# Performance work log

Measured on AMD Instinct MI355X. Metric: run time of the kernel, lower is better.

The kernel has to match this reference:

```python
import jax, jax.numpy as jnp
import numpy as np

C = 256
R = 16
K = 7

def setup_inputs() -> dict:
    key = jax.random.key(0)
    k1, k2, k3, k4 = jax.random.split(key, 4)
    x = jax.random.normal(k1, (16, C, 128, 128), dtype=jnp.float32)
    # PyTorch Linear weights: w1 [C//R, C], w2 [C, C//R]
    w1 = jax.random.normal(k2, (C // R, C), dtype=jnp.float32) * (1.0 / np.sqrt(C))
    w2 = jax.random.normal(k3, (C, C // R), dtype=jnp.float32) * (1.0 / np.sqrt(C // R))
    # Conv2d(2,1,K) weight: [out=1, in=2, K, K]
    wconv = jax.random.normal(k4, (1, 2, K, K), dtype=jnp.float32) * (1.0 / np.sqrt(2 * K * K))
    return {"x": x, "w1": w1, "w2": w2, "wconv": wconv}

def _mlp(v, w1, w2):  # v: [B, C]
    h = jax.nn.relu(v @ w1.T)  # [B, C//R]
    return h @ w2.T            # [B, C]

def reference(x, w1, w2, wconv):
    # channel attention
    avg = jnp.mean(x, axis=(2, 3))  # [B, C]
    mx = jnp.max(x, axis=(2, 3))    # [B, C]
    ch_att = jax.nn.sigmoid(_mlp(avg, w1, w2) + _mlp(mx, w1, w2))  # [B, C]
    x = x * ch_att[:, :, None, None]
    # spatial attention
    avg_sp = jnp.mean(x, axis=1, keepdims=True)  # [B,1,H,W]
    max_sp = jnp.max(x, axis=1, keepdims=True)   # [B,1,H,W]
    sp = jnp.concatenate([avg_sp, max_sp], axis=1)  # [B,2,H,W]
    conv = jax.lax.conv_general_dilated(
        sp, wconv, window_strides=(1, 1), padding=[(K // 2, K // 2)] * 2,
        dimension_numbers=("NCHW", "OIHW", "NCHW"))  # [B,1,H,W]
    sp_att = jax.nn.sigmoid(conv)
    return x * sp_att
```

## Files before the change

### kernel.cpp

```cpp
#include <hip/hip_runtime.h>
#include <hip/hip_fp16.h>
#include <math.h>

#define B   16
#define C   256
#define HW  16384
#define HW4 4096
#define HW8 2048
#define NCHUNK 4

typedef float vf4 __attribute__((ext_vector_type(4)));
typedef unsigned int vu4 __attribute__((ext_vector_type(4)));
typedef unsigned int vu2 __attribute__((ext_vector_type(2)));

__device__ __forceinline__ float2 h2f(unsigned int w) {
    __half2 h = *(const __half2*)&w;
    return __half22float2(h);
}

__device__ __forceinline__ float wave_reduce_sum(float v) {
    #pragma unroll
    for (int o = 32; o > 0; o >>= 1) v += __shfl_down(v, o, 64);
    return v;
}
__device__ __forceinline__ float wave_reduce_max(float v) {
    #pragma unroll
    for (int o = 32; o > 0; o >>= 1) v = fmaxf(v, __shfl_down(v, o, 64));
    return v;
}

__global__ __launch_bounds__(256) void k_chan_stats_cast(const float* __restrict__ x,
                                                         vu2* __restrict__ x16,
                                                         float* __restrict__ avg,
                                                         float* __restrict__ mx) {
    const int bc  = blockIdx.x;
    const int tid = threadIdx.x;
    const vf4* x4 = (const vf4*)x + (size_t)bc * HW4;
    vu2* o = x16 + (size_t)bc * HW4;
    float s = 0.f, m = -INFINITY;
    #pragma unroll
    for (int i = 0; i < 16; ++i) {
        vf4 v = __builtin_nontemporal_load(&x4[tid + i * 256]);
        s += (v.x + v.y) + (v.z + v.w);
        m = fmaxf(m, fmaxf(fmaxf(v.x, v.y), fmaxf(v.z, v.w)));
        __half2 lo = __halves2half2(__float2half_rn(v.x), __float2half_rn(v.y));
        __half2 hi = __halves2half2(__float2half_rn(v.z), __float2half_rn(v.w));
        vu2 u;
        u.x = *(const unsigned int*)&lo;
        u.y = *(const unsigned int*)&hi;
        o[tid + i * 256] = u;
    }
    s = wave_reduce_sum(s);
    m = wave_reduce_max(m);
    __shared__ float ss[4], sm[4];
    const int wid = tid >> 6, lane = tid & 63;
    if (lane == 0) { ss[wid] = s; sm[wid] = m; }
    __syncthreads();
    if (tid == 0) {
        float S = ss[0] + ss[1] + ss[2] + ss[3];
        float M = fmaxf(fmaxf(sm[0], sm[1]), fmaxf(sm[2], sm[3]));
        avg[bc] = S * (1.0f / HW);
        mx[bc]  = M;
    }
}

__global__ __launch_bounds__(256) void k_mlp(const float* __restrict__ avg,
                                             const float* __restrict__ mx,
                                             const float* __restrict__ w1,
                                             const float* __restrict__ w2,
                                             float* __restrict__ chatt) {
    const int b = blockIdx.x, tid = threadIdx.x;
    __shared__ float sa[C], sx[C], h[16];
    sa[tid] = avg[b * C + tid];
    sx[tid] = mx[b * C + tid];
    __syncthreads();
    const int j = tid >> 4, sub = tid & 15;
    float pa = 0.f, pm = 0.f;
    #pragma unroll
    for (int c2 = sub; c2 < C; c2 += 16) {
        float w = w1[j * C + c2];
        pa += sa[c2] * w;
        pm += sx[c2] * w;
    }
    #pragma unroll
    for (int o = 8; o > 0; o >>= 1) {
        pa += __shfl_down(pa, o, 16);
        pm += __shfl_down(pm, o, 16);
    }
    if (sub == 0) h[j] = fmaxf(pa, 0.f) + fmaxf(pm, 0.f);
    __syncthreads();
    float o = 0.f;
    #pragma unroll
    for (int jj = 0; jj < 16; ++jj) o += h[jj] * w2[tid * 16 + jj];
    chatt[b * C + tid] = 1.0f / (1.0f + expf(-o));
}

__global__ __launch_bounds__(256) void k_sp_partial(const vu4* __restrict__ x16,
                                                    const float* __restrict__ chatt,
                                                    float* __restrict__ pavg,
                                                    float* __restrict__ pmax) {
    const int blk   = blockIdx.x;
    const int chunk = blk & 3;
    const int tile  = (blk >> 2) & 7;
    const int b     = blk >> 5;
    const int tid   = threadIdx.x;
    const int g     = tile * 256 + tid;
    float s[8];
    float m[8];
    #pragma unroll
    for (int k = 0; k < 8; ++k) { s[k] = 0.f; m[k] = -INFINITY; }
    const int c0 = chunk * 64;
    #pragma unroll 4
    for (int c = c0; c < c0 + 64; ++c) {
        vu4 u = x16[((size_t)(b * C + c)) * HW8 + g];
        const float a = chatt[b * C + c];
        #pragma unroll
        for (int q = 0; q < 4; ++q) {
            float2 f = h2f(u[q]);
            float y0 = f.x * a, y1 = f.y * a;
            s[2*q]   += y0;  s[2*q+1] += y1;
            m[2*q]   = fmaxf(m[2*q],   y0);
            m[2*q+1] = fmaxf(m[2*q+1], y1);
        }
    }
    vf4* pa = (vf4*)(pavg + ((size_t)(chunk * B + b)) * HW + g * 8);
    vf4* pm = (vf4*)(pmax + ((size_t)(chunk * B + b)) * HW + g * 8);
    vf4 a0 = {s[0], s[1], s[2], s[3]};
    vf4 a1 = {s[4], s[5], s[6], s[7]};
    vf4 m0 = {m[0], m[1], m[2], m[3]};
    vf4 m1 = {m[4], m[5], m[6], m[7]};
    pa[0] = a0; pa[1] = a1;
    pm[0] = m0; pm[1] = m1;
}

__global__ __launch_bounds__(256) void k_comb_conv(const float* __restrict__ pavg,
                                                   const float* __restrict__ pmax,
                                                   const float* __restrict__ wc,
                                                   float* __restrict__ spatt) {
    const int blk = blockIdx.x;
    const int tx = blk & 7, ty = (blk >> 3) & 7, b = blk >> 6;
    __shared__ float sa[22][24], sm[22][24], swc[98];
    if (threadIdx.x < 98) swc[threadIdx.x] = wc[threadIdx.x];
    for (int idx = threadIdx.x; idx < 484; idx += 256) {
        const int ly = idx / 22, lx = idx - ly * 22;
        const int gy = ty * 16 + ly - 3, gx = tx * 16 + lx - 3;
        float s = 0.f, m = 0.f;
        if (gy >= 0 && gy < 128 && gx >= 0 && gx < 128) {
            const int p = gy * 128 + gx;
            float mm = -INFINITY;
            float ss = 0.f;
            #pragma unroll
            for (int ch = 0; ch < NCHUNK; ++ch) {
                ss += pavg[(size_t)(ch * B + b) * HW + p];
                mm = fmaxf(mm, pmax[(size_t)(ch * B + b) * HW + p]);
            }
            s = ss * (1.0f / C);
            m = mm;
        }
        sa[ly][lx] = s;
        sm[ly][lx] = m;
    }
    __syncthreads();
    const int px = threadIdx.x & 15, py = threadIdx.x >> 4;
    float acc = 0.f;
    #pragma unroll
    for (int kh = 0; kh < 7; ++kh) {
        #pragma unroll
        for (int kw = 0; kw < 7; ++kw) {
            acc += sa[py + kh][px + kw] * swc[kh * 7 + kw]
                 + sm[py + kh][px + kw] * swc[49 + kh * 7 + kw];
        }
    }
    spatt[(size_t)b * HW + (ty * 16 + py) * 128 + tx * 16 + px] =
        1.0f / (1.0f + expf(-acc));
}

__global__ __launch_bounds__(256) void k_final(const vu4* __restrict__ x16,
                                               const float* __restrict__ chatt,
                                               const vf4* __restrict__ spatt,
                                               vf4* __restrict__ out) {
    const size_t total  = (size_t)B * C * HW8;
    const size_t stride = (size_t)gridDim.x * 256;
    for (size_t f = (size_t)blockIdx.x * 256 + threadIdx.x; f < total; f += stride) {
        const size_t bc = f >> 11;
        const size_t g  = f & 2047;
        const size_t b  = bc >> 8;
        vu4 u = __builtin_nontemporal_load(&x16[f]);
        const float a = chatt[bc];
        vf4 sp0 = spatt[b * HW4 + g * 2];
        vf4 sp1 = spatt[b * HW4 + g * 2 + 1];
        float2 f0 = h2f(u.x);
        float2 f1 = h2f(u.y);
        float2 f2 = h2f(u.z);
        float2 f3 = h2f(u.w);
        vf4 r0, r1;
        r0.x = f0.x * a * sp0.x;  r0.y = f0.y * a * sp0.y;
        r0.z = f1.x * a * sp0.z;  r0.w = f1.y * a * sp0.w;
        r1.x = f2.x * a * sp1.x;  r1.y = f2.y * a * sp1.y;
        r1.z = f3.x * a * sp1.z;  r1.w = f3.y * a * sp1.w;
        __builtin_nontemporal_store(r0, &out[f * 2]);
        __builtin_nontemporal_store(r1, &out[f * 2 + 1]);
    }
}

extern "C" void kernel_launch(void* const* d_in, const int* in_sizes, int n_in,
                              void* d_out, int out_size, void* d_ws, size_t ws_size,
                              hipStream_t stream) {
    const float* x  = (const float*)d_in[0];
    const float* w1 = (const float*)d_in[1];
    const float* w2 = (const float*)d_in[2];
    const float* wc = (const float*)d_in[3];
    vf4* out = (vf4*)d_out;
    char* ws = (char*)d_ws;

    vu2* x16  = (vu2*)ws;
    char* p = ws + (size_t)B * C * HW * 2;
    float* avg   = (float*)p;            p += 4096 * 4;
    float* mx    = (float*)p;            p += 4096 * 4;
    float* chatt = (float*)p;            p += 4096 * 4;
    float* pavg  = (float*)p;            p += (size_t)NCHUNK * B * HW * 4;
    float* pmax  = (float*)p;            p += (size_t)NCHUNK * B * HW * 4;
    float* spatt = (float*)p;            p += (size_t)B * HW * 4;

    k_chan_stats_cast<<<B * C, 256, 0, stream>>>(x, x16, avg, mx);
    k_mlp<<<B, 256, 0, stream>>>(avg, mx, w1, w2, chatt);
    k_sp_partial<<<512, 256, 0, stream>>>((const vu4*)x16, chatt, pavg, pmax);
    k_comb_conv<<<1024, 256, 0, stream>>>(pavg, pmax, wc, spatt);
    k_final<<<4096, 256, 0, stream>>>((const vu4*)x16, chatt,
                                      (const vf4*)spatt, (vf4*)out);
}
```

Before: 209.8 us.

## Fuse all CBAM stages into one persistent kernel with grid barriers

```diff
diff --git a/kernel.cpp b/kernel.cpp
--- a/kernel.cpp
+++ b/kernel.cpp
@@ -8,6 +8,7 @@
 #define HW4 4096
 #define HW8 2048
 #define NCHUNK 4
+#define NBLK 512
 
 typedef float vf4 __attribute__((ext_vector_type(4)));
 typedef unsigned int vu4 __attribute__((ext_vector_type(4)));
@@ -29,177 +30,203 @@
     return v;
 }
 
-__global__ __launch_bounds__(256) void k_chan_stats_cast(const float* __restrict__ x,
-                                                         vu2* __restrict__ x16,
-                                                         float* __restrict__ avg,
-                                                         float* __restrict__ mx) {
-    const int bc  = blockIdx.x;
+__device__ __forceinline__ void gbar(unsigned* bar) {
+    __syncthreads();
+    if (threadIdx.x == 0) {
+        __threadfence();
+        unsigned g = __hip_atomic_load(&bar[32], __ATOMIC_RELAXED, __HIP_MEMORY_SCOPE_AGENT);
+        unsigned a = __hip_atomic_fetch_add(&bar[0], 1u, __ATOMIC_ACQ_REL, __HIP_MEMORY_SCOPE_AGENT);
+        if (a == NBLK - 1) {
+            __hip_atomic_store(&bar[0], 0u, __ATOMIC_RELAXED, __HIP_MEMORY_SCOPE_AGENT);
+            __hip_atomic_store(&bar[32], g + 1u, __ATOMIC_RELEASE, __HIP_MEMORY_SCOPE_AGENT);
+        } else {
+            while (__hip_atomic_load(&bar[32], __ATOMIC_ACQUIRE, __HIP_MEMORY_SCOPE_AGENT) == g)
+                __builtin_amdgcn_s_sleep(2);
+        }
+        __threadfence();
+    }
+    __syncthreads();
+}
+
+__global__ __launch_bounds__(256, 2) void k_cbam_fused(
+        const float* __restrict__ x,
+        const float* __restrict__ w1,
+        const float* __restrict__ w2,
+        const float* __restrict__ wc,
+        vu2*  __restrict__ x16,
+        float* __restrict__ avg, float* __restrict__ mx,
+        float* __restrict__ chatt,
+        float* __restrict__ pavg, float* __restrict__ pmax,
+        float* __restrict__ spatt,
+        vf4* __restrict__ out,
+        unsigned* __restrict__ bar) {
     const int tid = threadIdx.x;
-    const vf4* x4 = (const vf4*)x + (size_t)bc * HW4;
-    vu2* o = x16 + (size_t)bc * HW4;
-    float s = 0.f, m = -INFINITY;
-    #pragma unroll
-    for (int i = 0; i < 16; ++i) {
-        vf4 v = __builtin_nontemporal_load(&x4[tid + i * 256]);
-        s += (v.x + v.y) + (v.z + v.w);
-        m = fmaxf(m, fmaxf(fmaxf(v.x, v.y), fmaxf(v.z, v.w)));
-        __half2 lo = __halves2half2(__float2half_rn(v.x), __float2half_rn(v.y));
-        __half2 hi = __halves2half2(__float2half_rn(v.z), __float2half_rn(v.w));
-        vu2 u;
-        u.x = *(const unsigned int*)&lo;
-        u.y = *(const unsigned int*)&hi;
-        o[tid + i * 256] = u;
-    }
-    s = wave_reduce_sum(s);
-    m = wave_reduce_max(m);
-    __shared__ float ss[4], sm[4];
-    const int wid = tid >> 6, lane = tid & 63;
-    if (lane == 0) { ss[wid] = s; sm[wid] = m; }
-    __syncthreads();
-    if (tid == 0) {
-        float S = ss[0] + ss[1] + ss[2] + ss[3];
-        float M = fmaxf(fmaxf(sm[0], sm[1]), fmaxf(sm[2], sm[3]));
-        avg[bc] = S * (1.0f / HW);
-        mx[bc]  = M;
-    }
-}
-
-__global__ __launch_bounds__(256) void k_mlp(const float* __restrict__ avg,
-                                             const float* __restrict__ mx,
-                                             const float* __restrict__ w1,
-                                             const float* __restrict__ w2,
-                                             float* __restrict__ chatt) {
-    const int b = blockIdx.x, tid = threadIdx.x;
-    __shared__ float sa[C], sx[C], h[16];
-    sa[tid] = avg[b * C + tid];
-    sx[tid] = mx[b * C + tid];
-    __syncthreads();
-    const int j = tid >> 4, sub = tid & 15;
-    float pa = 0.f, pm = 0.f;
-    #pragma unroll
-    for (int c2 = sub; c2 < C; c2 += 16) {
-        float w = w1[j * C + c2];
-        pa += sa[c2] * w;
-        pm += sx[c2] * w;
-    }
-    #pragma unroll
-    for (int o = 8; o > 0; o >>= 1) {
-        pa += __shfl_down(pa, o, 16);
-        pm += __shfl_down(pm, o, 16);
-    }
-    if (sub == 0) h[j] = fmaxf(pa, 0.f) + fmaxf(pm, 0.f);
-    __syncthreads();
-    float o = 0.f;
-    #pragma unroll
-    for (int jj = 0; jj < 16; ++jj) o += h[jj] * w2[tid * 16 + jj];
-    chatt[b * C + tid] = 1.0f / (1.0f + expf(-o));
-}
-
-__global__ __launch_bounds__(256) void k_sp_partial(const vu4* __restrict__ x16,
-                                                    const float* __restrict__ chatt,
-                                                    float* __restrict__ pavg,
-                                                    float* __restrict__ pmax) {
-    const int blk   = blockIdx.x;
-    const int chunk = blk & 3;
-    const int tile  = (blk >> 2) & 7;
-    const int b     = blk >> 5;
-    const int tid   = threadIdx.x;
-    const int g     = tile * 256 + tid;
-    float s[8];
-    float m[8];
-    #pragma unroll
-    for (int k = 0; k < 8; ++k) { s[k] = 0.f; m[k] = -INFINITY; }
-    const int c0 = chunk * 64;
-    #pragma unroll 4
-    for (int c = c0; c < c0 + 64; ++c) {
-        vu4 u = x16[((size_t)(b * C + c)) * HW8 + g];
-        const float a = chatt[b * C + c];
-        #pragma unroll
-        for (int q = 0; q < 4; ++q) {
-            float2 f = h2f(u[q]);
-            float y0 = f.x * a, y1 = f.y * a;
-            s[2*q]   += y0;  s[2*q+1] += y1;
-            m[2*q]   = fmaxf(m[2*q],   y0);
-            m[2*q+1] = fmaxf(m[2*q+1], y1);
-        }
-    }
-    vf4* pa = (vf4*)(pavg + ((size_t)(chunk * B + b)) * HW + g * 8);
-    vf4* pm = (vf4*)(pmax + ((size_t)(chunk * B + b)) * HW + g * 8);
-    vf4 a0 = {s[0], s[1], s[2], s[3]};
-    vf4 a1 = {s[4], s[5], s[6], s[7]};
-    vf4 m0 = {m[0], m[1], m[2], m[3]};
-    vf4 m1 = {m[4], m[5], m[6], m[7]};
-    pa[0] = a0; pa[1] = a1;
-    pm[0] = m0; pm[1] = m1;
-}
-
-__global__ __launch_bounds__(256) void k_comb_conv(const float* __restrict__ pavg,
-                                                   const float* __restrict__ pmax,
-                                                   const float* __restrict__ wc,
-                                                   float* __restrict__ spatt) {
     const int blk = blockIdx.x;
-    const int tx = blk & 7, ty = (blk >> 3) & 7, b = blk >> 6;
-    __shared__ float sa[22][24], sm[22][24], swc[98];
-    if (threadIdx.x < 98) swc[threadIdx.x] = wc[threadIdx.x];
-    for (int idx = threadIdx.x; idx < 484; idx += 256) {
-        const int ly = idx / 22, lx = idx - ly * 22;
-        const int gy = ty * 16 + ly - 3, gx = tx * 16 + lx - 3;
-        float s = 0.f, m = 0.f;
-        if (gy >= 0 && gy < 128 && gx >= 0 && gx < 128) {
-            const int p = gy * 128 + gx;
-            float mm = -INFINITY;
-            float ss = 0.f;
+
+    __shared__ union {
+        struct { float sa[22][24]; float sm[22][24]; float wcs[98]; } conv;
+        struct { float sa[C]; float sx[C]; float h[16]; } mlp;
+        struct { float ss[4]; float sm[4]; } red;
+    } sh;
+
+    for (int k = 0; k < 8; ++k) {
+        const int bc = blk + k * NBLK;
+        const vf4* x4 = (const vf4*)x + (size_t)bc * HW4;
+        vu2* o = x16 + (size_t)bc * HW4;
+        float s = 0.f, m = -INFINITY;
+        #pragma unroll
+        for (int i = 0; i < 16; ++i) {
+            vf4 v = __builtin_nontemporal_load(&x4[tid + i * 256]);
+            s += (v.x + v.y) + (v.z + v.w);
+            m = fmaxf(m, fmaxf(fmaxf(v.x, v.y), fmaxf(v.z, v.w)));
+            __half2 lo = __halves2half2(__float2half_rn(v.x), __float2half_rn(v.y));
+            __half2 hi = __halves2half2(__float2half_rn(v.z), __float2half_rn(v.w));
+            vu2 u;
+            u.x = *(const unsigned int*)&lo;
+            u.y = *(const unsigned int*)&hi;
+            o[tid + i * 256] = u;
+        }
+        s = wave_reduce_sum(s);
+        m = wave_reduce_max(m);
+        const int wid = tid >> 6, lane = tid & 63;
+        if (lane == 0) { sh.red.ss[wid] = s; sh.red.sm[wid] = m; }
+        __syncthreads();
+        if (tid == 0) {
+            float S = sh.red.ss[0] + sh.red.ss[1] + sh.red.ss[2] + sh.red.ss[3];
+            float M = fmaxf(fmaxf(sh.red.sm[0], sh.red.sm[1]),
+                            fmaxf(sh.red.sm[2], sh.red.sm[3]));
+            avg[bc] = S * (1.0f / HW);
+            mx[bc]  = M;
+        }
+        __syncthreads();
+    }
+    gbar(bar);
+
+    if (blk < B) {
+        const int b = blk;
+        sh.mlp.sa[tid] = avg[b * C + tid];
+        sh.mlp.sx[tid] = mx[b * C + tid];
+        __syncthreads();
+        const int j = tid >> 4, sub = tid & 15;
+        float pa = 0.f, pm = 0.f;
+        #pragma unroll
+        for (int c2 = sub; c2 < C; c2 += 16) {
+            float w = w1[j * C + c2];
+            pa += sh.mlp.sa[c2] * w;
+            pm += sh.mlp.sx[c2] * w;
+        }
+        #pragma unroll
+        for (int o = 8; o > 0; o >>= 1) {
+            pa += __shfl_down(pa, o, 16);
+            pm += __shfl_down(pm, o, 16);
+        }
+        if (sub == 0) sh.mlp.h[j] = fmaxf(pa, 0.f) + fmaxf(pm, 0.f);
+        __syncthreads();
+        float o = 0.f;
+        #pragma unroll
+        for (int jj = 0; jj < 16; ++jj) o += sh.mlp.h[jj] * w2[tid * 16 + jj];
+        chatt[b * C + tid] = 1.0f / (1.0f + expf(-o));
+    }
+    gbar(bar);
+
+    {
+        const int chunk = blk & 3;
+        const int tile  = (blk >> 2) & 7;
+        const int b     = blk >> 5;
+        const int g     = tile * 256 + tid;
+        const vu4* xx = (const vu4*)x16;
+        float s[8], m[8];
+        #pragma unroll
+        for (int k = 0; k < 8; ++k) { s[k] = 0.f; m[k] = -INFINITY; }
+        const int c0 = chunk * 64;
+        #pragma unroll 4
+        for (int c = c0; c < c0 + 64; ++c) {
+            vu4 u = xx[((size_t)(b * C + c)) * HW8 + g];
+            const float a = chatt[b * C + c];
             #pragma unroll
-            for (int ch = 0; ch < NCHUNK; ++ch) {
-                ss += pavg[(size_t)(ch * B + b) * HW + p];
-                mm = fmaxf(mm, pmax[(size_t)(ch * B + b) * HW + p]);
+            for (int q = 0; q < 4; ++q) {
+                float2 f = h2f(u[q]);
+                float y0 = f.x * a, y1 = f.y * a;
+                s[2*q]   += y0;  s[2*q+1] += y1;
+                m[2*q]   = fmaxf(m[2*q],   y0);
+                m[2*q+1] = fmaxf(m[2*q+1], y1);
             }
-            s = ss * (1.0f / C);
-            m = mm;
-        }
-        sa[ly][lx] = s;
-        sm[ly][lx] = m;
-    }
-    __syncthreads();
-    const int px = threadIdx.x & 15, py = threadIdx.x >> 4;
-    float acc = 0.f;
-    #pragma unroll
-    for (int kh = 0; kh < 7; ++kh) {
-        #pragma unroll
-        for (int kw = 0; kw < 7; ++kw) {
-            acc += sa[py + kh][px + kw] * swc[kh * 7 + kw]
-                 + sm[py + kh][px + kw] * swc[49 + kh * 7 + kw];
-        }
-    }
-    spatt[(size_t)b * HW + (ty * 16 + py) * 128 + tx * 16 + px] =
-        1.0f / (1.0f + expf(-acc));
-}
-
-__global__ __launch_bounds__(256) void k_final(const vu4* __restrict__ x16,
-                                               const float* __restrict__ chatt,
-                                               const vf4* __restrict__ spatt,
-                                               vf4* __restrict__ out) {
-    const size_t total  = (size_t)B * C * HW8;
-    const size_t stride = (size_t)gridDim.x * 256;
-    for (size_t f = (size_t)blockIdx.x * 256 + threadIdx.x; f < total; f += stride) {
-        const size_t bc = f >> 11;
-        const size_t g  = f & 2047;
-        const size_t b  = bc >> 8;
-        vu4 u = __builtin_nontemporal_load(&x16[f]);
-        const float a = chatt[bc];
-        vf4 sp0 = spatt[b * HW4 + g * 2];
-        vf4 sp1 = spatt[b * HW4 + g * 2 + 1];
-        float2 f0 = h2f(u.x);
-        float2 f1 = h2f(u.y);
-        float2 f2 = h2f(u.z);
-        float2 f3 = h2f(u.w);
-        vf4 r0, r1;
-        r0.x = f0.x * a * sp0.x;  r0.y = f0.y * a * sp0.y;
-        r0.z = f1.x * a * sp0.z;  r0.w = f1.y * a * sp0.w;
-        r1.x = f2.x * a * sp1.x;  r1.y = f2.y * a * sp1.y;
-        r1.z = f3.x * a * sp1.z;  r1.w = f3.y * a * sp1.w;
-        __builtin_nontemporal_store(r0, &out[f * 2]);
-        __builtin_nontemporal_store(r1, &out[f * 2 + 1]);
+        }
+        vf4* pa = (vf4*)(pavg + ((size_t)(chunk * B + b)) * HW + g * 8);
+        vf4* pm = (vf4*)(pmax + ((size_t)(chunk * B + b)) * HW + g * 8);
+        vf4 a0 = {s[0], s[1], s[2], s[3]};
+        vf4 a1 = {s[4], s[5], s[6], s[7]};
+        vf4 m0 = {m[0], m[1], m[2], m[3]};
+        vf4 m1 = {m[4], m[5], m[6], m[7]};
+        pa[0] = a0; pa[1] = a1;
+        pm[0] = m0; pm[1] = m1;
+    }
+    gbar(bar);
+
+    for (int t = 0; t < 2; ++t) {
+        const int tj = blk + t * NBLK;
+        const int tx = tj & 7, ty = (tj >> 3) & 7, b = tj >> 6;
+        if (tid < 98) sh.conv.wcs[tid] = wc[tid];
+        for (int idx = tid; idx < 484; idx += 256) {
+            const int ly = idx / 22, lx = idx - ly * 22;
+            const int gy = ty * 16 + ly - 3, gx = tx * 16 + lx - 3;
+            float s = 0.f, m = 0.f;
+            if (gy >= 0 && gy < 128 && gx >= 0 && gx < 128) {
+                const int p = gy * 128 + gx;
+                float mm = -INFINITY, ss = 0.f;
+                #pragma unroll
+                for (int ch = 0; ch < NCHUNK; ++ch) {
+                    ss += pavg[(size_t)(ch * B + b) * HW + p];
+                    mm = fmaxf(mm, pmax[(size_t)(ch * B + b) * HW + p]);
+                }
+                s = ss * (1.0f / C);
+                m = mm;
+            }
+            sh.conv.sa[ly][lx] = s;
+            sh.conv.sm[ly][lx] = m;
+        }
+        __syncthreads();
+        const int px = tid & 15, py = tid >> 4;
+        float acc = 0.f;
+        #pragma unroll
+        for (int kh = 0; kh < 7; ++kh) {
+            #pragma unroll
+            for (int kw = 0; kw < 7; ++kw) {
+                acc += sh.conv.sa[py + kh][px + kw] * sh.conv.wcs[kh * 7 + kw]
+                     + sh.conv.sm[py + kh][px + kw] * sh.conv.wcs[49 + kh * 7 + kw];
+            }
+        }
+        spatt[(size_t)b * HW + (ty * 16 + py) * 128 + tx * 16 + px] =
+            1.0f / (1.0f + expf(-acc));
+        __syncthreads();
+    }
+    gbar(bar);
+
+    {
+        const vu4* xx = (const vu4*)x16;
+        const vf4* sp4 = (const vf4*)spatt;
+        const size_t total  = (size_t)B * C * HW8;
+        const size_t stride = (size_t)NBLK * 256;
+        for (size_t f = (size_t)blk * 256 + tid; f < total; f += stride) {
+            const size_t bc = f >> 11;
+            const size_t g  = f & 2047;
+            const size_t b  = bc >> 8;
+            vu4 u = __builtin_nontemporal_load(&xx[f]);
+            const float a = chatt[bc];
+            vf4 sp0 = sp4[b * HW4 + g * 2];
+            vf4 sp1 = sp4[b * HW4 + g * 2 + 1];
+            float2 f0 = h2f(u.x);
+            float2 f1 = h2f(u.y);
+            float2 f2 = h2f(u.z);
+            float2 f3 = h2f(u.w);
+            vf4 r0, r1;
+            r0.x = f0.x * a * sp0.x;  r0.y = f0.y * a * sp0.y;
+            r0.z = f1.x * a * sp0.z;  r0.w = f1.y * a * sp0.w;
+            r1.x = f2.x * a * sp1.x;  r1.y = f2.y * a * sp1.y;
+            r1.z = f3.x * a * sp1.z;  r1.w = f3.y * a * sp1.w;
+            __builtin_nontemporal_store(r0, &out[f * 2]);
+            __builtin_nontemporal_store(r1, &out[f * 2 + 1]);
+        }
     }
 }
 
@@ -221,11 +248,9 @@
     float* pavg  = (float*)p;            p += (size_t)NCHUNK * B * HW * 4;
     float* pmax  = (float*)p;            p += (size_t)NCHUNK * B * HW * 4;
     float* spatt = (float*)p;            p += (size_t)B * HW * 4;
-
-    k_chan_stats_cast<<<B * C, 256, 0, stream>>>(x, x16, avg, mx);
-    k_mlp<<<B, 256, 0, stream>>>(avg, mx, w1, w2, chatt);
-    k_sp_partial<<<512, 256, 0, stream>>>((const vu4*)x16, chatt, pavg, pmax);
-    k_comb_conv<<<1024, 256, 0, stream>>>(pavg, pmax, wc, spatt);
-    k_final<<<4096, 256, 0, stream>>>((const vu4*)x16, chatt,
-                                      (const vf4*)spatt, (vf4*)out);
-}
+    unsigned* bar = (unsigned*)p;
+    hipMemsetAsync(bar, 0, 256, stream);
+
+    k_cbam_fused<<<NBLK, 256, 0, stream>>>(x, w1, w2, wc, x16, avg, mx, chatt,
+                                           pavg, pmax, spatt, out, bar);
+}
```

New measurement: 464.6 us. +121.4%, slower.

## Fuse channel MLP into spatial-partial and final kernels, double channel chunks

Applied to the files above, without the earlier changes.

```diff
diff --git a/kernel.cpp b/kernel.cpp
--- a/kernel.cpp
+++ b/kernel.cpp
@@ -7,7 +7,7 @@
 #define HW  16384
 #define HW4 4096
 #define HW8 2048
-#define NCHUNK 4
+#define NCHUNK 8
 
 typedef float vf4 __attribute__((ext_vector_type(4)));
 typedef unsigned int vu4 __attribute__((ext_vector_type(4)));
@@ -27,6 +27,31 @@
     #pragma unroll
     for (int o = 32; o > 0; o >>= 1) v = fmaxf(v, __shfl_down(v, o, 64));
     return v;
+}
+
+__device__ __forceinline__ void mlp_hidden(const float* __restrict__ avg,
+                                           const float* __restrict__ mx,
+                                           const float* __restrict__ w1,
+                                           int b, int tid,
+                                           float* sa, float* sx, float* h) {
+    sa[tid] = avg[b * C + tid];
+    sx[tid] = mx[b * C + tid];
+    __syncthreads();
+    const int j = tid >> 4, sub = tid & 15;
+    float pa = 0.f, pm = 0.f;
+    #pragma unroll
+    for (int c2 = sub; c2 < C; c2 += 16) {
+        float w = w1[j * C + c2];
+        pa += sa[c2] * w;
+        pm += sx[c2] * w;
+    }
+    #pragma unroll
+    for (int o = 8; o > 0; o >>= 1) {
+        pa += __shfl_down(pa, o, 16);
+        pm += __shfl_down(pm, o, 16);
+    }
+    if (sub == 0) h[j] = fmaxf(pa, 0.f) + fmaxf(pm, 0.f);
+    __syncthreads();
 }
 
 __global__ __launch_bounds__(256) void k_chan_stats_cast(const float* __restrict__ x,
@@ -64,63 +89,58 @@
     }
 }
 
-__global__ __launch_bounds__(256) void k_mlp(const float* __restrict__ avg,
-                                             const float* __restrict__ mx,
-                                             const float* __restrict__ w1,
-                                             const float* __restrict__ w2,
-                                             float* __restrict__ chatt) {
-    const int b = blockIdx.x, tid = threadIdx.x;
-    __shared__ float sa[C], sx[C], h[16];
-    sa[tid] = avg[b * C + tid];
-    sx[tid] = mx[b * C + tid];
-    __syncthreads();
-    const int j = tid >> 4, sub = tid & 15;
-    float pa = 0.f, pm = 0.f;
-    #pragma unroll
-    for (int c2 = sub; c2 < C; c2 += 16) {
-        float w = w1[j * C + c2];
-        pa += sa[c2] * w;
-        pm += sx[c2] * w;
-    }
-    #pragma unroll
-    for (int o = 8; o > 0; o >>= 1) {
-        pa += __shfl_down(pa, o, 16);
-        pm += __shfl_down(pm, o, 16);
-    }
-    if (sub == 0) h[j] = fmaxf(pa, 0.f) + fmaxf(pm, 0.f);
-    __syncthreads();
-    float o = 0.f;
-    #pragma unroll
-    for (int jj = 0; jj < 16; ++jj) o += h[jj] * w2[tid * 16 + jj];
-    chatt[b * C + tid] = 1.0f / (1.0f + expf(-o));
-}
-
-__global__ __launch_bounds__(256) void k_sp_partial(const vu4* __restrict__ x16,
-                                                    const float* __restrict__ chatt,
-                                                    float* __restrict__ pavg,
-                                                    float* __restrict__ pmax) {
+__global__ __launch_bounds__(256, 4) void k_sp_partial(const vu4* __restrict__ x16,
+                                                       const float* __restrict__ avg,
+                                                       const float* __restrict__ mx,
+                                                       const float* __restrict__ w1,
+                                                       const float* __restrict__ w2,
+                                                       float* __restrict__ pavg,
+                                                       float* __restrict__ pmax) {
     const int blk   = blockIdx.x;
-    const int chunk = blk & 3;
-    const int tile  = (blk >> 2) & 7;
-    const int b     = blk >> 5;
+    const int chunk = blk & 7;
+    const int tile  = (blk >> 3) & 7;
+    const int b     = blk >> 6;
     const int tid   = threadIdx.x;
-    const int g     = tile * 256 + tid;
-    float s[8];
-    float m[8];
+
+    __shared__ float sa[C], sx[C], h[16], att[32];
+    mlp_hidden(avg, mx, w1, b, tid, sa, sx, h);
+    if (tid < 32) {
+        const int c = chunk * 32 + tid;
+        float o = 0.f;
+        #pragma unroll
+        for (int jj = 0; jj < 16; ++jj) o += h[jj] * w2[c * 16 + jj];
+        att[tid] = 1.0f / (1.0f + expf(-o));
+    }
+    __syncthreads();
+
+    const int g = tile * 256 + tid;
+    const vu4* base = x16 + ((size_t)(b * C + chunk * 32)) * HW8 + g;
+    float s[8], m[8];
     #pragma unroll
     for (int k = 0; k < 8; ++k) { s[k] = 0.f; m[k] = -INFINITY; }
-    const int c0 = chunk * 64;
-    #pragma unroll 4
-    for (int c = c0; c < c0 + 64; ++c) {
-        vu4 u = x16[((size_t)(b * C + c)) * HW8 + g];
-        const float a = chatt[b * C + c];
+    #pragma unroll 2
+    for (int cc = 0; cc < 32; cc += 4) {
+        vu4 u0 = base[(size_t)(cc + 0) * HW8];
+        vu4 u1 = base[(size_t)(cc + 1) * HW8];
+        vu4 u2 = base[(size_t)(cc + 2) * HW8];
+        vu4 u3 = base[(size_t)(cc + 3) * HW8];
+        const float a0 = att[cc + 0], a1 = att[cc + 1];
+        const float a2 = att[cc + 2], a3 = att[cc + 3];
         #pragma unroll
         for (int q = 0; q < 4; ++q) {
-            float2 f = h2f(u[q]);
-            float y0 = f.x * a, y1 = f.y * a;
-            s[2*q]   += y0;  s[2*q+1] += y1;
-            m[2*q]   = fmaxf(m[2*q],   y0);
-            m[2*q+1] = fmaxf(m[2*q+1], y1);
+            float2 f0 = h2f(u0[q]);
+            float2 f1 = h2f(u1[q]);
+            float2 f2 = h2f(u2[q]);
+            float2 f3 = h2f(u3[q]);
+            float y;
+            y = f0.x * a0; s[2*q] += y; m[2*q] = fmaxf(m[2*q], y);
+            y = f1.x * a1; s[2*q] += y; m[2*q] = fmaxf(m[2*q], y);
+            y = f2.x * a2; s[2*q] += y; m[2*q] = fmaxf(m[2*q], y);
+            y = f3.x * a3; s[2*q] += y; m[2*q] = fmaxf(m[2*q], y);
+            y = f0.y * a0; s[2*q+1] += y; m[2*q+1] = fmaxf(m[2*q+1], y);
+            y = f1.y * a1; s[2*q+1] += y; m[2*q+1] = fmaxf(m[2*q+1], y);
+            y = f2.y * a2; s[2*q+1] += y; m[2*q+1] = fmaxf(m[2*q+1], y);
+            y = f3.y * a3; s[2*q+1] += y; m[2*q+1] = fmaxf(m[2*q+1], y);
         }
     }
     vf4* pa = (vf4*)(pavg + ((size_t)(chunk * B + b)) * HW + g * 8);
@@ -176,19 +196,38 @@
 }
 
 __global__ __launch_bounds__(256) void k_final(const vu4* __restrict__ x16,
-                                               const float* __restrict__ chatt,
+                                               const float* __restrict__ avg,
+                                               const float* __restrict__ mx,
+                                               const float* __restrict__ w1,
+                                               const float* __restrict__ w2,
                                                const vf4* __restrict__ spatt,
                                                vf4* __restrict__ out) {
-    const size_t total  = (size_t)B * C * HW8;
-    const size_t stride = (size_t)gridDim.x * 256;
-    for (size_t f = (size_t)blockIdx.x * 256 + threadIdx.x; f < total; f += stride) {
-        const size_t bc = f >> 11;
-        const size_t g  = f & 2047;
-        const size_t b  = bc >> 8;
-        vu4 u = __builtin_nontemporal_load(&x16[f]);
-        const float a = chatt[bc];
-        vf4 sp0 = spatt[b * HW4 + g * 2];
-        vf4 sp1 = spatt[b * HW4 + g * 2 + 1];
+    const int bc  = blockIdx.x;
+    const int b   = bc >> 8;
+    const int c   = bc & 255;
+    const int tid = threadIdx.x;
+
+    __shared__ float sa[C], sx[C], h[16];
+    __shared__ float attc;
+    mlp_hidden(avg, mx, w1, b, tid, sa, sx, h);
+    if (tid == 0) {
+        float o = 0.f;
+        #pragma unroll
+        for (int jj = 0; jj < 16; ++jj) o += h[jj] * w2[c * 16 + jj];
+        attc = 1.0f / (1.0f + expf(-o));
+    }
+    __syncthreads();
+    const float a = attc;
+
+    const vu4* xx = x16 + (size_t)bc * HW8;
+    const vf4* sp = spatt + (size_t)b * HW4;
+    vf4* ob = out + (size_t)bc * HW4;
+    #pragma unroll
+    for (int i = 0; i < 8; ++i) {
+        const int g = i * 256 + tid;
+        vu4 u = __builtin_nontemporal_load(&xx[g]);
+        vf4 sp0 = sp[g * 2];
+        vf4 sp1 = sp[g * 2 + 1];
         float2 f0 = h2f(u.x);
         float2 f1 = h2f(u.y);
         float2 f2 = h2f(u.z);
@@ -198,8 +237,8 @@
         r0.z = f1.x * a * sp0.z;  r0.w = f1.y * a * sp0.w;
         r1.x = f2.x * a * sp1.x;  r1.y = f2.y * a * sp1.y;
         r1.z = f3.x * a * sp1.z;  r1.w = f3.y * a * sp1.w;
-        __builtin_nontemporal_store(r0, &out[f * 2]);
-        __builtin_nontemporal_store(r1, &out[f * 2 + 1]);
+        __builtin_nontemporal_store(r0, &ob[g * 2]);
+        __builtin_nontemporal_store(r1, &ob[g * 2 + 1]);
     }
 }
 
@@ -217,15 +256,14 @@
     char* p = ws + (size_t)B * C * HW * 2;
     float* avg   = (float*)p;            p += 4096 * 4;
     float* mx    = (float*)p;            p += 4096 * 4;
-    float* chatt = (float*)p;            p += 4096 * 4;
     float* pavg  = (float*)p;            p += (size_t)NCHUNK * B * HW * 4;
     float* pmax  = (float*)p;            p += (size_t)NCHUNK * B * HW * 4;
     float* spatt = (float*)p;            p += (size_t)B * HW * 4;
 
     k_chan_stats_cast<<<B * C, 256, 0, stream>>>(x, x16, avg, mx);
-    k_mlp<<<B, 256, 0, stream>>>(avg, mx, w1, w2, chatt);
-    k_sp_partial<<<512, 256, 0, stream>>>((const vu4*)x16, chatt, pavg, pmax);
+    k_sp_partial<<<1024, 256, 0, stream>>>((const vu4*)x16, avg, mx, w1, w2,
+                                           pavg, pmax);
     k_comb_conv<<<1024, 256, 0, stream>>>(pavg, pmax, wc, spatt);
-    k_final<<<4096, 256, 0, stream>>>((const vu4*)x16, chatt,
-                                      (const vf4*)spatt, (vf4*)out);
-}
+    k_final<<<B * C, 256, 0, stream>>>((const vu4*)x16, avg, mx, w1, w2,
+                                       (const vf4*)spatt, (vf4*)out);
+}
```

Measured after the change: 248.4 us. 18.4% more time.

## Restructure final scale kernel to reuse spatial attention across channel groups

Applied to the files above, without the earlier changes.

```diff
diff --git a/kernel.cpp b/kernel.cpp
--- a/kernel.cpp
+++ b/kernel.cpp
@@ -179,27 +179,42 @@
                                                const float* __restrict__ chatt,
                                                const vf4* __restrict__ spatt,
                                                vf4* __restrict__ out) {
-    const size_t total  = (size_t)B * C * HW8;
-    const size_t stride = (size_t)gridDim.x * 256;
-    for (size_t f = (size_t)blockIdx.x * 256 + threadIdx.x; f < total; f += stride) {
-        const size_t bc = f >> 11;
-        const size_t g  = f & 2047;
-        const size_t b  = bc >> 8;
-        vu4 u = __builtin_nontemporal_load(&x16[f]);
-        const float a = chatt[bc];
-        vf4 sp0 = spatt[b * HW4 + g * 2];
-        vf4 sp1 = spatt[b * HW4 + g * 2 + 1];
-        float2 f0 = h2f(u.x);
-        float2 f1 = h2f(u.y);
-        float2 f2 = h2f(u.z);
-        float2 f3 = h2f(u.w);
-        vf4 r0, r1;
-        r0.x = f0.x * a * sp0.x;  r0.y = f0.y * a * sp0.y;
-        r0.z = f1.x * a * sp0.z;  r0.w = f1.y * a * sp0.w;
-        r1.x = f2.x * a * sp1.x;  r1.y = f2.y * a * sp1.y;
-        r1.z = f3.x * a * sp1.z;  r1.w = f3.y * a * sp1.w;
-        __builtin_nontemporal_store(r0, &out[f * 2]);
-        __builtin_nontemporal_store(r1, &out[f * 2 + 1]);
+    const int blk  = blockIdx.x;
+    const int cg   = blk & 7;
+    const int tile = (blk >> 3) & 7;
+    const int b    = blk >> 6;
+    const int tid  = threadIdx.x;
+    const int g    = tile * 256 + tid;
+
+    __shared__ float att[32];
+    if (tid < 32) att[tid] = chatt[b * C + cg * 32 + tid];
+    __syncthreads();
+
+    const vf4 sp0 = spatt[(size_t)b * HW4 + g * 2];
+    const vf4 sp1 = spatt[(size_t)b * HW4 + g * 2 + 1];
+
+    const vu4* xb = x16 + ((size_t)(b * C + cg * 32)) * HW8 + g;
+    vf4* ob = out + ((size_t)(b * C + cg * 32)) * HW4 + (size_t)g * 2;
+
+    for (int cc = 0; cc < 32; cc += 8) {
+        vu4 u[8];
+        #pragma unroll
+        for (int k = 0; k < 8; ++k)
+            u[k] = __builtin_nontemporal_load(&xb[(size_t)(cc + k) * HW8]);
+        #pragma unroll
+        for (int k = 0; k < 8; ++k) {
+            const float a = att[cc + k];
+            float2 f0 = h2f(u[k].x);
+            float2 f1 = h2f(u[k].y);
+            float2 f2 = h2f(u[k].z);
+            float2 f3 = h2f(u[k].w);
+            vf4 r0 = {f0.x * a * sp0.x, f0.y * a * sp0.y,
+                      f1.x * a * sp0.z, f1.y * a * sp0.w};
+            vf4 r1 = {f2.x * a * sp1.x, f2.y * a * sp1.y,
+                      f3.x * a * sp1.z, f3.y * a * sp1.w};
+            __builtin_nontemporal_store(r0, &ob[(size_t)(cc + k) * HW4]);
+            __builtin_nontemporal_store(r1, &ob[(size_t)(cc + k) * HW4 + 1]);
+        }
     }
 }
 
@@ -226,6 +241,6 @@
     k_mlp<<<B, 256, 0, stream>>>(avg, mx, w1, w2, chatt);
     k_sp_partial<<<512, 256, 0, stream>>>((const vu4*)x16, chatt, pavg, pmax);
     k_comb_conv<<<1024, 256, 0, stream>>>(pavg, pmax, wc, spatt);
-    k_final<<<4096, 256, 0, stream>>>((const vu4*)x16, chatt,
+    k_final<<<1024, 256, 0, stream>>>((const vu4*)x16, chatt,
                                       (const vf4*)spatt, (vf4*)out);
 }
```

New measurement: 252.3 us. 1.2x slower.
